# Optimization experiments

Hardware: AMD Instinct MI355X
Metric: run time of the kernel (lower is better)

The kernel has to match this reference:

```python
import jax, jax.numpy as jnp
import numpy as np

NA, NPAP = 50000, 100000
D_IN, D_HID, D_OUT = 512, 512, 256
E_AP, E_PA, E_AA = 400000, 400000, 200000
NEG_SLOPE = 0.2


def setup_inputs() -> dict:
    key = jax.random.key(0)
    ks = jax.random.split(key, 18)
    f32 = jnp.float32

    def edges(k, e, n_src, n_dst):
        k1, k2 = jax.random.split(k)
        return jnp.stack([
            jax.random.randint(k1, (e,), 0, n_src),
            jax.random.randint(k2, (e,), 0, n_dst),
        ]).astype(jnp.int64)

    return {
        'x_author': jax.random.normal(ks[0], (NA, D_IN), f32),
        'x_paper': jax.random.normal(ks[1], (NPAP, D_IN), f32),
        # layer 1 params
        'W1': jax.random.normal(ks[2], (2, D_IN, D_HID), f32) / np.sqrt(D_IN),
        'b1': jnp.zeros((2, D_HID), f32),
        'att1': jax.random.normal(ks[3], (3, 2, D_HID), f32) * 0.1,
        'kW1': jax.random.normal(ks[4], (D_HID, D_HID), f32) / np.sqrt(D_HID),
        'kb1': jnp.zeros((D_HID,), f32),
        'q1': jax.random.normal(ks[5], (D_HID,), f32) * 0.1,
        # layer 2 params
        'W2': jax.random.normal(ks[6], (2, D_HID, D_OUT), f32) / np.sqrt(D_HID),
        'b2': jnp.zeros((2, D_OUT), f32),
        'att2': jax.random.normal(ks[7], (3, 2, D_OUT), f32) * 0.1,
        'kW2': jax.random.normal(ks[8], (D_OUT, D_OUT), f32) / np.sqrt(D_OUT),
        'kb2': jnp.zeros((D_OUT,), f32),
        'q2': jax.random.normal(ks[9], (D_OUT,), f32) * 0.1,
        # edge index dict: (author,writes,paper), (paper,written_by,author), (author,coauthor,author)
        'e_ap': edges(ks[10], E_AP, NA, NPAP),
        'e_pa': edges(ks[11], E_PA, NPAP, NA),
        'e_aa': edges(ks[12], E_AA, NA, NA),
    }


def _edge_type_attn(h_src, h_dst, a_src, a_dst, ei, n_dst):
    """One edge-type GAT-style aggregation of HANConv (heads=1)."""
    src, dst = ei[0], ei[1]
    alpha = (h_src @ a_src)[src] + (h_dst @ a_dst)[dst]        # [E]
    alpha = jax.nn.leaky_relu(alpha, NEG_SLOPE)
    m = jax.ops.segment_max(alpha, dst, num_segments=n_dst)    # softmax over dst groups
    e = jnp.exp(alpha - m[dst])
    denom = jax.ops.segment_sum(e, dst, num_segments=n_dst)
    w = e / denom[dst]                                          # [E]
    out = jax.ops.segment_sum(h_src[src] * w[:, None], dst, num_segments=n_dst)
    return jax.nn.relu(out)                                     # [n_dst, D]


def _semantic_group(outs, kW, kb, q):
    """outs: [T, N, D]; semantic attention over T metapaths."""
    score = jnp.einsum('tnd,d->t', jnp.tanh(outs @ kW + kb), q) / outs.shape[1]
    attn = jax.nn.softmax(score)
    return jnp.einsum('t,tnd->nd', attn, outs)


def _han_layer(x_a, x_p, W, b, att, kW, kb, q, e_ap, e_pa, e_aa):
    h_a = x_a @ W[0] + b[0]   # per-node-type projection
    h_p = x_p @ W[1] + b[1]
    na, npap = h_a.shape[0], h_p.shape[0]
    out_p = _edge_type_attn(h_a, h_p, att[0, 0], att[0, 1], e_ap, npap)
    out_a1 = _edge_type_attn(h_p, h_a, att[1, 0], att[1, 1], e_pa, na)
    out_a2 = _edge_type_attn(h_a, h_a, att[2, 0], att[2, 1], e_aa, na)
    out_a = _semantic_group(jnp.stack([out_a1, out_a2]), kW, kb, q)
    out_p = _semantic_group(out_p[None], kW, kb, q)
    return out_a, out_p


def reference(x_author, x_paper, W1, b1, att1, kW1, kb1, q1,
              W2, b2, att2, kW2, kb2, q2, e_ap, e_pa, e_aa):
    h_a, h_p = _han_layer(x_author, x_paper, W1, b1, att1, kW1, kb1, q1, e_ap, e_pa, e_aa)
    h_a, h_p = _han_layer(h_a, h_p, W2, b2, att2, kW2, kb2, q2, e_ap, e_pa, e_aa)
    return h_a  # x['author']
```

## Files before the change

kernel.cpp:

```cpp
#include <hip/hip_runtime.h>
#include <hip/hip_bf16.h>

#define NA 50000
#define NPAP 100000
#define DIN 512
#define DHID 512
#define DOUT 256
#define EAP 400000
#define EPA 400000
#define EAA 200000

typedef unsigned short u16;
typedef __attribute__((ext_vector_type(8))) short bf16x8;
typedef __attribute__((ext_vector_type(4))) float f32x4;

__device__ inline float bflo(unsigned v) { return __uint_as_float(v << 16); }
__device__ inline float bfhi(unsigned v) { return __uint_as_float(v & 0xffff0000u); }
__device__ inline u16 f2bf_rne(float x) {
    unsigned u = __float_as_uint(x);
    return (u16)((u + 0x7FFFu + ((u >> 16) & 1u)) >> 16);
}
__device__ inline unsigned pack2bf(float a, float b) {
    return (unsigned)f2bf_rne(a) | ((unsigned)f2bf_rne(b) << 16);
}


__global__ void fill_u32_kernel(unsigned* __restrict__ p, unsigned v, int n) {
    int i = blockIdx.x * blockDim.x + threadIdx.x;
    if (i < n) p[i] = v;
}

__global__ void detect_kernel(const unsigned* __restrict__ e, int npairs, int* __restrict__ flag) {
    __shared__ int anyn;
    if (threadIdx.x == 0) anyn = 0;
    __syncthreads();
    unsigned local = 0;
    for (int i = threadIdx.x; i < npairs; i += blockDim.x) local |= e[2 * i + 1];
    if (local) atomicOr(&anyn, 1);
    __syncthreads();
    if (threadIdx.x == 0) flag[0] = (anyn == 0) ? 1 : 0;
}

__device__ inline int edge_at(const void* e, size_t idx, int i64) {
    return i64 ? (int)((const long long*)e)[idx] : ((const int*)e)[idx];
}


__global__ void conv_bt_kernel(const float* __restrict__ B, u16* __restrict__ bth,
                               u16* __restrict__ btl, int K, int N) {
    __shared__ float tile[32][33];
    const int nb = blockIdx.x * 32, kb = blockIdx.y * 32;
    const int tx = threadIdx.x, ty = threadIdx.y;
    const int KBLK = K >> 5;
    for (int i = ty; i < 32; i += 8)
        tile[i][tx] = B[(size_t)(kb + i) * N + nb + tx];
    __syncthreads();
    for (int i = ty; i < 32; i += 8) {
        float v = tile[tx][i];
        unsigned u = __float_as_uint(v);
        unsigned h = (u + 0x7FFFu + ((u >> 16) & 1u)) >> 16;
        float hf = __uint_as_float(h << 16);
        float r = v - hf;
        unsigned l = __float_as_uint(r) >> 16;
        const int n = nb + i, k = kb + tx;
        const int nblk = n >> 7, row = n & 127;
        const int kblk = k >> 5, kc = (k & 31) >> 3, ke = k & 7;
        const int cph = kc ^ ((row >> 1) & 3);
        size_t o = (((size_t)(nblk * KBLK + kblk) * 128 + row) << 5) + (cph << 3) + ke;
        bth[o] = (u16)h;
        btl[o] = (u16)l;
    }
}


template <bool BF16OUT>
__global__ __launch_bounds__(256, 4) void mfma_gemm_2p_kernel(
    const float* __restrict__ A,
    const u16* __restrict__ Bth, const u16* __restrict__ Btl,
    const float* __restrict__ bias,
    float* __restrict__ C, int M, int N, int K, int gx)
{
    __shared__ u16 Ah[128][32];
    __shared__ u16 Bh[128][32];
    __shared__ u16 Bl[128][32];

    const int nwg = gridDim.x;
    const int bid = blockIdx.x;
    const int qc = nwg >> 3, rc = nwg & 7;
    const int xcd = bid & 7, idx = bid >> 3;
    const int wg = (xcd < rc ? xcd * (qc + 1) : rc * (qc + 1) + (xcd - rc) * qc) + idx;
    const int bx = wg % gx, by = wg / gx;
    const int m0 = by * 128;
    const int n0 = bx * 128;

    const int tid = threadIdx.x;
    const int lane = tid & 63;
    const int wv = tid >> 6;
    const int wm = wv >> 1, wn = wv & 1;
    const int fr = lane & 15;
    const int kg = lane >> 4;

    const int srow = tid >> 1;
    const int oh   = tid & 1;
    const bool a_ok = (m0 + srow) < M;
    const float* Ap = A + (size_t)(m0 + srow) * K + oh * 16;

    const int swc = (srow >> 1) & 3;
    const int p0 = srow * 32 + ((((oh << 1) + 0) ^ swc) << 3);
    const int p1 = srow * 32 + ((((oh << 1) + 1) ^ swc) << 3);
    const int rdc = (kg ^ ((fr >> 1) & 3)) << 3;

    const int KBLK = K >> 5;
    const size_t btile0 = ((size_t)(n0 >> 7) * KBLK) << 12;
    const int bso0 = wv * 512 + lane * 8;
    const int bso1 = (wv + 4) * 512 + lane * 8;

    f32x4 acc[4][4] = {};

    const int nt = K >> 5;
    for (int t = 0; t < nt; ++t) {
        __syncthreads();
        {
            const int k0 = t << 5;
            uint4 w0 = make_uint4(0, 0, 0, 0), w1 = w0;
            if (a_ok) {
                float ar[16];
#pragma unroll
                for (int c4 = 0; c4 < 4; ++c4) {
                    float4 v = *(const float4*)(Ap + k0 + c4 * 4);
                    ar[c4 * 4 + 0] = v.x; ar[c4 * 4 + 1] = v.y;
                    ar[c4 * 4 + 2] = v.z; ar[c4 * 4 + 3] = v.w;
                }
                w0 = make_uint4(pack2bf(ar[0], ar[1]), pack2bf(ar[2], ar[3]),
                                pack2bf(ar[4], ar[5]), pack2bf(ar[6], ar[7]));
                w1 = make_uint4(pack2bf(ar[8], ar[9]), pack2bf(ar[10], ar[11]),
                                pack2bf(ar[12], ar[13]), pack2bf(ar[14], ar[15]));
            }
            const u16* bt = Bth + btile0 + ((size_t)t << 12);
            const u16* blt = Btl + btile0 + ((size_t)t << 12);
            uint4 bh0 = *(const uint4*)(bt + bso0);
            uint4 bh1 = *(const uint4*)(bt + bso1);
            uint4 bl0 = *(const uint4*)(blt + bso0);
            uint4 bl1 = *(const uint4*)(blt + bso1);

            u16* ahp = &Ah[0][0];
            *(uint4*)&ahp[p0] = w0;
            *(uint4*)&ahp[p1] = w1;
            u16* bhp = &Bh[0][0];
            u16* blp = &Bl[0][0];
            *(uint4*)&bhp[bso0] = bh0;
            *(uint4*)&bhp[bso1] = bh1;
            *(uint4*)&blp[bso0] = bl0;
            *(uint4*)&blp[bso1] = bl1;
        }
        __syncthreads();

        bf16x8 afh[4], bfh[4], bfl[4];
#pragma unroll
        for (int i = 0; i < 4; ++i) {
            const int aoff = (wm * 64 + i * 16 + fr) * 32 + rdc;
            const int boff = (wn * 64 + i * 16 + fr) * 32 + rdc;
            afh[i] = *(const bf16x8*)&Ah[0][aoff];
            bfh[i] = *(const bf16x8*)&Bh[0][boff];
            bfl[i] = *(const bf16x8*)&Bl[0][boff];
        }
#pragma unroll
        for (int i = 0; i < 4; ++i)
#pragma unroll
            for (int j = 0; j < 4; ++j) {
                acc[i][j] = __builtin_amdgcn_mfma_f32_16x16x32_bf16(afh[i], bfh[j], acc[i][j], 0, 0, 0);
                acc[i][j] = __builtin_amdgcn_mfma_f32_16x16x32_bf16(afh[i], bfl[j], acc[i][j], 0, 0, 0);
            }
    }

#pragma unroll
    for (int j = 0; j < 4; ++j) {
        const int col = n0 + wn * 64 + j * 16 + fr;
        const float bj = bias[col];
#pragma unroll
        for (int i = 0; i < 4; ++i) {
            const int rbase = m0 + wm * 64 + i * 16 + kg * 4;
#pragma unroll
            for (int r = 0; r < 4; ++r) {
                const int grow = rbase + r;
                if (grow < M) {
                    if (BF16OUT)
                        ((u16*)C)[(size_t)grow * N + col] = f2bf_rne(acc[i][j][r] + bj);
                    else
                        C[(size_t)grow * N + col] = acc[i][j][r] + bj;
                }
            }
        }
    }
}


template <bool COMB, bool BF16OUT>
__global__ __launch_bounds__(256, 4) void mfma_gemm_bfA_kernel(
    const u16* __restrict__ A, const u16* __restrict__ A2,
    const float* __restrict__ cwp,
    const u16* __restrict__ Bth, const u16* __restrict__ Btl,
    const float* __restrict__ bias,
    float* __restrict__ C, int M, int N, int K, int gx)
{
    __shared__ u16 Ah[128][32];
    __shared__ u16 Bh[128][32];
    __shared__ u16 Bl[128][32];

    const int nwg = gridDim.x;
    const int bid = blockIdx.x;
    const int qc = nwg >> 3, rc = nwg & 7;
    const int xcd = bid & 7, idx = bid >> 3;
    const int wg = (xcd < rc ? xcd * (qc + 1) : rc * (qc + 1) + (xcd - rc) * qc) + idx;
    const int bx = wg % gx, by = wg / gx;
    const int m0 = by * 128;
    const int n0 = bx * 128;

    const int tid = threadIdx.x;
    const int lane = tid & 63;
    const int wv = tid >> 6;
    const int wm = wv >> 1, wn = wv & 1;
    const int fr = lane & 15;
    const int kg = lane >> 4;

    const int srow = tid >> 1;
    const int oh   = tid & 1;
    const bool a_ok = (m0 + srow) < M;
    const u16* Ap  = A + (size_t)(m0 + srow) * K + oh * 16;
    const u16* Ap2 = COMB ? (A2 + (size_t)(m0 + srow) * K + oh * 16) : nullptr;
    float cw0 = 1.f, cw1 = 0.f;
    if (COMB) { cw0 = cwp[0]; cw1 = cwp[1]; }

    const int swc = (srow >> 1) & 3;
    const int p0 = srow * 32 + ((((oh << 1) + 0) ^ swc) << 3);
    const int p1 = srow * 32 + ((((oh << 1) + 1) ^ swc) << 3);
    const int rdc = (kg ^ ((fr >> 1) & 3)) << 3;

    const int KBLK = K >> 5;
    const size_t btile0 = ((size_t)(n0 >> 7) * KBLK) << 12;
    const int bso0 = wv * 512 + lane * 8;
    const int bso1 = (wv + 4) * 512 + lane * 8;

    f32x4 acc[4][4] = {};

    const int nt = K >> 5;
    for (int t = 0; t < nt; ++t) {
        __syncthreads();
        {
            const int k0 = t << 5;
            uint4 a0 = make_uint4(0, 0, 0, 0), a1 = a0;
            if (a_ok) {
                a0 = *(const uint4*)(Ap + k0);
                a1 = *(const uint4*)(Ap + k0 + 8);
                if (COMB) {
                    uint4 c0 = *(const uint4*)(Ap2 + k0);
                    uint4 c1 = *(const uint4*)(Ap2 + k0 + 8);
                    a0.x = pack2bf(cw0 * bflo(a0.x) + cw1 * bflo(c0.x), cw0 * bfhi(a0.x) + cw1 * bfhi(c0.x));
                    a0.y = pack2bf(cw0 * bflo(a0.y) + cw1 * bflo(c0.y), cw0 * bfhi(a0.y) + cw1 * bfhi(c0.y));
                    a0.z = pack2bf(cw0 * bflo(a0.z) + cw1 * bflo(c0.z), cw0 * bfhi(a0.z) + cw1 * bfhi(c0.z));
                    a0.w = pack2bf(cw0 * bflo(a0.w) + cw1 * bflo(c0.w), cw0 * bfhi(a0.w) + cw1 * bfhi(c0.w));
                    a1.x = pack2bf(cw0 * bflo(a1.x) + cw1 * bflo(c1.x), cw0 * bfhi(a1.x) + cw1 * bfhi(c1.x));
                    a1.y = pack2bf(cw0 * bflo(a1.y) + cw1 * bflo(c1.y), cw0 * bfhi(a1.y) + cw1 * bfhi(c1.y));
                    a1.z = pack2bf(cw0 * bflo(a1.z) + cw1 * bflo(c1.z), cw0 * bfhi(a1.z) + cw1 * bfhi(c1.z));
                    a1.w = pack2bf(cw0 * bflo(a1.w) + cw1 * bflo(c1.w), cw0 * bfhi(a1.w) + cw1 * bfhi(c1.w));
                }
            }
            const u16* bt = Bth + btile0 + ((size_t)t << 12);
            const u16* blt = Btl + btile0 + ((size_t)t << 12);
            uint4 bh0 = *(const uint4*)(bt + bso0);
            uint4 bh1 = *(const uint4*)(bt + bso1);
            uint4 bl0 = *(const uint4*)(blt + bso0);
            uint4 bl1 = *(const uint4*)(blt + bso1);

            u16* ahp = &Ah[0][0];
            *(uint4*)&ahp[p0] = a0;
            *(uint4*)&ahp[p1] = a1;
            u16* bhp = &Bh[0][0];
            u16* blp = &Bl[0][0];
            *(uint4*)&bhp[bso0] = bh0;
            *(uint4*)&bhp[bso1] = bh1;
            *(uint4*)&blp[bso0] = bl0;
            *(uint4*)&blp[bso1] = bl1;
        }
        __syncthreads();

        bf16x8 afh[4], bfh[4], bfl[4];
#pragma unroll
        for (int i = 0; i < 4; ++i) {
            const int aoff = (wm * 64 + i * 16 + fr) * 32 + rdc;
            const int boff = (wn * 64 + i * 16 + fr) * 32 + rdc;
            afh[i] = *(const bf16x8*)&Ah[0][aoff];
            bfh[i] = *(const bf16x8*)&Bh[0][boff];
            bfl[i] = *(const bf16x8*)&Bl[0][boff];
        }
#pragma unroll
        for (int i = 0; i < 4; ++i)
#pragma unroll
            for (int j = 0; j < 4; ++j) {
                acc[i][j] = __builtin_amdgcn_mfma_f32_16x16x32_bf16(afh[i], bfh[j], acc[i][j], 0, 0, 0);
                acc[i][j] = __builtin_amdgcn_mfma_f32_16x16x32_bf16(afh[i], bfl[j], acc[i][j], 0, 0, 0);
            }
    }

#pragma unroll
    for (int j = 0; j < 4; ++j) {
        const int col = n0 + wn * 64 + j * 16 + fr;
        const float bj = bias[col];
#pragma unroll
        for (int i = 0; i < 4; ++i) {
            const int rbase = m0 + wm * 64 + i * 16 + kg * 4;
#pragma unroll
            for (int r = 0; r < 4; ++r) {
                const int grow = rbase + r;
                if (grow < M) {
                    if (BF16OUT)
                        ((u16*)C)[(size_t)grow * N + col] = f2bf_rne(acc[i][j][r] + bj);
                    else
                        C[(size_t)grow * N + col] = acc[i][j][r] + bj;
                }
            }
        }
    }
}


template <bool BF16A>
__global__ __launch_bounds__(256, 4) void mfma_score1_kernel(
    const void* __restrict__ A_, const u16* __restrict__ Bth,
    const float* __restrict__ bias, int M, int N, int K,
    const float* __restrict__ qv, float* __restrict__ score, int gx)
{
    __shared__ u16 Ah[128][32];
    __shared__ u16 Bh[128][32];

    const int nwg = gridDim.x;
    const int bid = blockIdx.x;
    const int qc = nwg >> 3, rc = nwg & 7;
    const int xcd = bid & 7, idx = bid >> 3;
    const int wg = (xcd < rc ? xcd * (qc + 1) : rc * (qc + 1) + (xcd - rc) * qc) + idx;
    const int bx = wg % gx, by = wg / gx;
    const int m0 = by * 128;
    const int n0 = bx * 128;

    const int tid = threadIdx.x;
    const int lane = tid & 63;
    const int wv = tid >> 6;
    const int wm = wv >> 1, wn = wv & 1;
    const int fr = lane & 15;
    const int kg = lane >> 4;

    const int srow = tid >> 1;
    const int oh   = tid & 1;
    const bool a_ok = (m0 + srow) < M;

    const int swc = (srow >> 1) & 3;
    const int p0 = srow * 32 + ((((oh << 1) + 0) ^ swc) << 3);
    const int p1 = srow * 32 + ((((oh << 1) + 1) ^ swc) << 3);
    const int rdc = (kg ^ ((fr >> 1) & 3)) << 3;

    const int KBLK = K >> 5;
    const size_t btile0 = ((size_t)(n0 >> 7) * KBLK) << 12;
    const int bso0 = wv * 512 + lane * 8;
    const int bso1 = (wv + 4) * 512 + lane * 8;

    f32x4 acc[4][4] = {};

    const int nt = K >> 5;
    for (int t = 0; t < nt; ++t) {
        __syncthreads();
        {
            const int k0 = t << 5;
            uint4 w0 = make_uint4(0, 0, 0, 0), w1 = w0;
            if (a_ok) {
                if (BF16A) {
                    const u16* Ap = (const u16*)A_ + (size_t)(m0 + srow) * K + oh * 16;
                    w0 = *(const uint4*)(Ap + k0);
                    w1 = *(const uint4*)(Ap + k0 + 8);
                } else {
                    const float* Ap = (const float*)A_ + (size_t)(m0 + srow) * K + oh * 16;
                    float ar[16];
#pragma unroll
                    for (int c4 = 0; c4 < 4; ++c4) {
                        float4 v = *(const float4*)(Ap + k0 + c4 * 4);
                        ar[c4 * 4 + 0] = v.x; ar[c4 * 4 + 1] = v.y;
                        ar[c4 * 4 + 2] = v.z; ar[c4 * 4 + 3] = v.w;
                    }
                    w0 = make_uint4(pack2bf(ar[0], ar[1]), pack2bf(ar[2], ar[3]),
                                    pack2bf(ar[4], ar[5]), pack2bf(ar[6], ar[7]));
                    w1 = make_uint4(pack2bf(ar[8], ar[9]), pack2bf(ar[10], ar[11]),
                                    pack2bf(ar[12], ar[13]), pack2bf(ar[14], ar[15]));
                }
            }
            const u16* bt = Bth + btile0 + ((size_t)t << 12);
            uint4 bh0 = *(const uint4*)(bt + bso0);
            uint4 bh1 = *(const uint4*)(bt + bso1);
            u16* ahp = &Ah[0][0];
            *(uint4*)&ahp[p0] = w0;
            *(uint4*)&ahp[p1] = w1;
            u16* bhp = &Bh[0][0];
            *(uint4*)&bhp[bso0] = bh0;
            *(uint4*)&bhp[bso1] = bh1;
        }
        __syncthreads();

        bf16x8 afh[4], bfh[4];
#pragma unroll
        for (int i = 0; i < 4; ++i) {
            afh[i] = *(const bf16x8*)&Ah[0][(wm * 64 + i * 16 + fr) * 32 + rdc];
            bfh[i] = *(const bf16x8*)&Bh[0][(wn * 64 + i * 16 + fr) * 32 + rdc];
        }
#pragma unroll
        for (int i = 0; i < 4; ++i)
#pragma unroll
            for (int j = 0; j < 4; ++j)
                acc[i][j] = __builtin_amdgcn_mfma_f32_16x16x32_bf16(afh[i], bfh[j], acc[i][j], 0, 0, 0);
    }

    float ssum = 0.f;
#pragma unroll
    for (int j = 0; j < 4; ++j) {
        const int col = n0 + wn * 64 + j * 16 + fr;
        const float bj = bias[col];
        const float qj = qv[col];
#pragma unroll
        for (int i = 0; i < 4; ++i) {
            const int rbase = m0 + wm * 64 + i * 16 + kg * 4;
#pragma unroll
            for (int r = 0; r < 4; ++r) {
                if (rbase + r < M) ssum += tanhf(acc[i][j][r] + bj) * qj;
            }
        }
    }
#pragma unroll
    for (int o = 32; o; o >>= 1) ssum += __shfl_xor(ssum, o);
    __syncthreads();
    float* red = (float*)&Ah[0][0];
    if (lane == 0) red[wv] = ssum;
    __syncthreads();
    if (tid == 0) atomicAdd(score, red[0] + red[1] + red[2] + red[3]);
}


template <int NV, bool BF16IN>
__global__ void scores_kernel(const void* __restrict__ h, int n, int D,
                              const float* __restrict__ v0, const float* __restrict__ v1,
                              const float* __restrict__ v2, const float* __restrict__ v3,
                              float* __restrict__ s0, float* __restrict__ s1,
                              float* __restrict__ s2, float* __restrict__ s3)
{
    const int lane = threadIdx.x & 63;
    int wid = (blockIdx.x * blockDim.x + threadIdx.x) >> 6;
    const int nw = (gridDim.x * blockDim.x) >> 6;
    for (int node = wid; node < n; node += nw) {
        float a0 = 0, a1 = 0, a2 = 0, a3 = 0;
        for (int d = lane * 4; d < D; d += 256) {
            float4 x;
            if (BF16IN) {
                const u16* row = (const u16*)h + (size_t)node * D;
                uint2 bv = *(const uint2*)&row[d];
                x = make_float4(bflo(bv.x), bfhi(bv.x), bflo(bv.y), bfhi(bv.y));
            } else {
                const float* row = (const float*)h + (size_t)node * D;
                x = *(const float4*)&row[d];
            }
            float4 w = *(const float4*)&v0[d];
            a0 += x.x * w.x + x.y * w.y + x.z * w.z + x.w * w.w;
            if (NV > 1) { float4 u = *(const float4*)&v1[d]; a1 += x.x * u.x + x.y * u.y + x.z * u.z + x.w * u.w; }
            if (NV > 2) { float4 u = *(const float4*)&v2[d]; a2 += x.x * u.x + x.y * u.y + x.z * u.z + x.w * u.w; }
            if (NV > 3) { float4 u = *(const float4*)&v3[d]; a3 += x.x * u.x + x.y * u.y + x.z * u.z + x.w * u.w; }
        }
#pragma unroll
        for (int o = 32; o; o >>= 1) {
            a0 += __shfl_xor(a0, o);
            if (NV > 1) a1 += __shfl_xor(a1, o);
            if (NV > 2) a2 += __shfl_xor(a2, o);
            if (NV > 3) a3 += __shfl_xor(a3, o);
        }
        if (lane == 0) {
            s0[node] = a0;
            if (NV > 1) s1[node] = a1;
            if (NV > 2) s2[node] = a2;
            if (NV > 3) s3[node] = a3;
        }
    }
}


__global__ void count3_kernel(const void* __restrict__ eA, const void* __restrict__ eB,
                              const void* __restrict__ eC, const int* __restrict__ flag,
                              int* __restrict__ cA, int* __restrict__ cB, int* __restrict__ cC) {
    int i = blockIdx.x * blockDim.x + threadIdx.x;
    int f = *flag;
    if (i < EAP) {
        atomicAdd(&cA[edge_at(eA, (size_t)EAP + i, f)], 1);
    } else if (i < EAP + EPA) {
        int j = i - EAP;
        atomicAdd(&cB[edge_at(eB, (size_t)EPA + j, f)], 1);
    } else if (i < EAP + EPA + EAA) {
        int j = i - EAP - EPA;
        atomicAdd(&cC[edge_at(eC, (size_t)EAA + j, f)], 1);
    }
}


__global__ void scanp1_kernel(const int* __restrict__ cnt, int n, int* __restrict__ part) {
    __shared__ int wsum[16];
    const int base = blockIdx.x * 1024;
    const int t = threadIdx.x, lane = t & 63, w = t >> 6;
    int v = (base + t < n) ? cnt[base + t] : 0;
#pragma unroll
    for (int o = 1; o < 64; o <<= 1) v += __shfl_xor(v, o);
    if (lane == 0) wsum[w] = v;
    __syncthreads();
    if (t == 0) {
        int s = 0;
#pragma unroll
        for (int k = 0; k < 16; ++k) s += wsum[k];
        part[blockIdx.x] = s;
    }
}

__global__ void scanp2_kernel(int* __restrict__ part, int nblk) {
    __shared__ int wsum[16];
    const int t = threadIdx.x, lane = t & 63, w = t >> 6;
    int v = (t < nblk) ? part[t] : 0;
    int x = v;
#pragma unroll
    for (int o = 1; o < 64; o <<= 1) { int y = __shfl_up(x, o); if (lane >= o) x += y; }
    if (lane == 63) wsum[w] = x;
    __syncthreads();
    if (w == 0 && lane < 16) {
        int s = wsum[lane];
#pragma unroll
        for (int o = 1; o < 16; o <<= 1) { int y = __shfl_up(s, o); if (lane >= o) s += y; }
        wsum[lane] = s;
    }
    __syncthreads();
    const int woff = (w > 0) ? wsum[w - 1] : 0;
    if (t < nblk) part[t] = woff + x - v;
}

__global__ void scanp3_kernel(const int* __restrict__ cnt, int n, const int* __restrict__ part,
                              int* __restrict__ offs_ap, int* __restrict__ cur_ap,
                              int* __restrict__ offs_pa, int* __restrict__ cur_pa,
                              int* __restrict__ offs_aa, int* __restrict__ cur_aa) {
    __shared__ int wsum[16];
    const int base = blockIdx.x * 1024;
    const int t = threadIdx.x, lane = t & 63, w = t >> 6;
    int v = (base + t < n) ? cnt[base + t] : 0;
    int x = v;
#pragma unroll
    for (int o = 1; o < 64; o <<= 1) { int y = __shfl_up(x, o); if (lane >= o) x += y; }
    if (lane == 63) wsum[w] = x;
    __syncthreads();
    if (w == 0 && lane < 16) {
        int s = wsum[lane];
#pragma unroll
        for (int o = 1; o < 16; o <<= 1) { int y = __shfl_up(s, o); if (lane >= o) s += y; }
        wsum[lane] = s;
    }
    __syncthreads();
    const int woff = (w > 0) ? wsum[w - 1] : 0;
    const int g = part[blockIdx.x] + woff + x - v;
    const int i = base + t;
    if (i < n) {
        if (i < NPAP)                 { offs_ap[i] = g; cur_ap[i] = g; }
        else if (i == NPAP)           { offs_ap[NPAP] = g; }
        else if (i < NPAP + 1 + NA)   { int j = i - NPAP - 1; int val = g - EAP; offs_pa[j] = val; cur_pa[j] = val; }
        else if (i == NPAP + 1 + NA)  { offs_pa[NA] = g - EAP; }
        else if (i < NPAP + 2 + 2*NA) { int j = i - NPAP - NA - 2; int val = g - EAP - EPA; offs_aa[j] = val; cur_aa[j] = val; }
        else                          { offs_aa[NA] = g - EAP - EPA; }
    }
}

__global__ void scatter3_kernel(const void* __restrict__ eA, const void* __restrict__ eB,
                                const void* __restrict__ eC, const int* __restrict__ flag,
                                int* __restrict__ uA, int* __restrict__ uB, int* __restrict__ uC,
                                int* __restrict__ idA, int* __restrict__ idB, int* __restrict__ idC) {
    int i = blockIdx.x * blockDim.x + threadIdx.x;
    int f = *flag;
    if (i < EAP) {
        int d = edge_at(eA, (size_t)EAP + i, f);
        idA[atomicAdd(&uA[d], 1)] = i;
    } else if (i < EAP + EPA) {
        int j = i - EAP;
        int d = edge_at(eB, (size_t)EPA + j, f);
        idB[atomicAdd(&uB[d], 1)] = j;
    } else if (i < EAP + EPA + EAA) {
        int j = i - EAP - EPA;
        int d = edge_at(eC, (size_t)EAA + j, f);
        idC[atomicAdd(&uC[d], 1)] = j;
    }
}


template <int DW, bool BF16H, bool BF16OUT>
__global__ __launch_bounds__(256) void agg_fused_kernel(
    const int* __restrict__ offs, const int* __restrict__ eids,
    const void* __restrict__ e, const int* __restrict__ flag,
    const float* __restrict__ ssrc, const float* __restrict__ sdst,
    const void* __restrict__ hsrc_, void* __restrict__ out,
    int n_dst, int E, int D)
{
    const int lane = threadIdx.x & 63;
    int wid = (blockIdx.x * blockDim.x + threadIdx.x) >> 6;
    const int nw = (gridDim.x * blockDim.x) >> 6;
    const int f = *flag;
    for (int dst = wid; dst < n_dst; dst += nw) {
        const int beg = offs[dst], end = offs[dst + 1];
        const float sd = sdst[dst];

        float dsum = 0.f;
        for (int j = beg + lane; j < end; j += 64) {
            int eid = eids[j];
            float a = ssrc[edge_at(e, eid, f)] + sd;
            a = (a >= 0.f) ? a : 0.2f * a;
            dsum += expf(a);
        }
#pragma unroll
        for (int o = 32; o; o >>= 1) dsum += __shfl_xor(dsum, o);
        const float rden = (end > beg) ? 1.f / dsum : 0.f;

        float acc[DW] = {};
        int j = beg;
        for (; j + 4 <= end; j += 4) {
            const int e0 = eids[j], e1 = eids[j + 1], e2 = eids[j + 2], e3 = eids[j + 3];
            const int q0 = edge_at(e, e0, f), q1 = edge_at(e, e1, f);
            const int q2 = edge_at(e, e2, f), q3 = edge_at(e, e3, f);
            float a0 = ssrc[q0] + sd, a1 = ssrc[q1] + sd;
            float a2 = ssrc[q2] + sd, a3 = ssrc[q3] + sd;
            a0 = (a0 >= 0.f) ? a0 : 0.2f * a0;
            a1 = (a1 >= 0.f) ? a1 : 0.2f * a1;
            a2 = (a2 >= 0.f) ? a2 : 0.2f * a2;
            a3 = (a3 >= 0.f) ? a3 : 0.2f * a3;
            const float w0 = expf(a0) * rden, w1 = expf(a1) * rden;
            const float w2 = expf(a2) * rden, w3 = expf(a3) * rden;
            if (BF16H) {
                const u16* hb = (const u16*)hsrc_;
                const u16* r0 = hb + (size_t)q0 * D + lane * DW;
                const u16* r1 = hb + (size_t)q1 * D + lane * DW;
                const u16* r2 = hb + (size_t)q2 * D + lane * DW;
                const u16* r3 = hb + (size_t)q3 * D + lane * DW;
                if constexpr (DW >= 8) {
#pragma unroll
                    for (int c = 0; c < DW; c += 8) {
                        uint4 b0 = *(const uint4*)&r0[c];
                        uint4 b1 = *(const uint4*)&r1[c];
                        uint4 b2 = *(const uint4*)&r2[c];
                        uint4 b3 = *(const uint4*)&r3[c];
                        acc[c + 0] += bflo(b0.x) * w0 + bflo(b1.x) * w1 + bflo(b2.x) * w2 + bflo(b3.x) * w3;
                        acc[c + 1] += bfhi(b0.x) * w0 + bfhi(b1.x) * w1 + bfhi(b2.x) * w2 + bfhi(b3.x) * w3;
                        acc[c + 2] += bflo(b0.y) * w0 + bflo(b1.y) * w1 + bflo(b2.y) * w2 + bflo(b3.y) * w3;
                        acc[c + 3] += bfhi(b0.y) * w0 + bfhi(b1.y) * w1 + bfhi(b2.y) * w2 + bfhi(b3.y) * w3;
                        acc[c + 4] += bflo(b0.z) * w0 + bflo(b1.z) * w1 + bflo(b2.z) * w2 + bflo(b3.z) * w3;
                        acc[c + 5] += bfhi(b0.z) * w0 + bfhi(b1.z) * w1 + bfhi(b2.z) * w2 + bfhi(b3.z) * w3;
                        acc[c + 6] += bflo(b0.w) * w0 + bflo(b1.w) * w1 + bflo(b2.w) * w2 + bflo(b3.w) * w3;
                        acc[c + 7] += bfhi(b0.w) * w0 + bfhi(b1.w) * w1 + bfhi(b2.w) * w2 + bfhi(b3.w) * w3;
                    }
                } else {
                    uint2 b0 = *(const uint2*)r0;
                    uint2 b1 = *(const uint2*)r1;
                    uint2 b2 = *(const uint2*)r2;
                    uint2 b3 = *(const uint2*)r3;
                    acc[0] += bflo(b0.x) * w0 + bflo(b1.x) * w1 + bflo(b2.x) * w2 + bflo(b3.x) * w3;
                    acc[1] += bfhi(b0.x) * w0 + bfhi(b1.x) * w1 + bfhi(b2.x) * w2 + bfhi(b3.x) * w3;
                    acc[2] += bflo(b0.y) * w0 + bflo(b1.y) * w1 + bflo(b2.y) * w2 + bflo(b3.y) * w3;
                    acc[3] += bfhi(b0.y) * w0 + bfhi(b1.y) * w1 + bfhi(b2.y) * w2 + bfhi(b3.y) * w3;
                }
            } else {
                const float* hf = (const float*)hsrc_;
                const float* r0 = hf + (size_t)q0 * D + lane * DW;
                const float* r1 = hf + (size_t)q1 * D + lane * DW;
                const float* r2 = hf + (size_t)q2 * D + lane * DW;
                const float* r3 = hf + (size_t)q3 * D + lane * DW;
#pragma unroll
                for (int c = 0; c < DW; c += 4) {
                    float4 a0v = *(const float4*)&r0[c];
                    float4 a1v = *(const float4*)&r1[c];
                    float4 a2v = *(const float4*)&r2[c];
                    float4 a3v = *(const float4*)&r3[c];
                    acc[c + 0] += a0v.x * w0 + a1v.x * w1 + a2v.x * w2 + a3v.x * w3;
                    acc[c + 1] += a0v.y * w0 + a1v.y * w1 + a2v.y * w2 + a3v.y * w3;
                    acc[c + 2] += a0v.z * w0 + a1v.z * w1 + a2v.z * w2 + a3v.z * w3;
                    acc[c + 3] += a0v.w * w0 + a1v.w * w1 + a2v.w * w2 + a3v.w * w3;
                }
            }
        }
        for (; j < end; ++j) {
            const int eid = eids[j];
            const int q = edge_at(e, eid, f);
            float a = ssrc[q] + sd;
            a = (a >= 0.f) ? a : 0.2f * a;
            const float w = expf(a) * rden;
            if (BF16H) {
                const u16* row = (const u16*)hsrc_ + (size_t)q * D + lane * DW;
                if constexpr (DW >= 8) {
#pragma unroll
                    for (int c = 0; c < DW; c += 8) {
                        uint4 b0 = *(const uint4*)&row[c];
                        acc[c + 0] += bflo(b0.x) * w; acc[c + 1] += bfhi(b0.x) * w;
                        acc[c + 2] += bflo(b0.y) * w; acc[c + 3] += bfhi(b0.y) * w;
                        acc[c + 4] += bflo(b0.z) * w; acc[c + 5] += bfhi(b0.z) * w;
                        acc[c + 6] += bflo(b0.w) * w; acc[c + 7] += bfhi(b0.w) * w;
                    }
                } else {
                    uint2 b0 = *(const uint2*)row;
                    acc[0] += bflo(b0.x) * w; acc[1] += bfhi(b0.x) * w;
                    acc[2] += bflo(b0.y) * w; acc[3] += bfhi(b0.y) * w;
                }
            } else {
                const float* row = (const float*)hsrc_ + (size_t)q * D + lane * DW;
#pragma unroll
                for (int c = 0; c < DW; c += 4) {
                    float4 v = *(const float4*)&row[c];
                    acc[c + 0] += v.x * w; acc[c + 1] += v.y * w;
                    acc[c + 2] += v.z * w; acc[c + 3] += v.w * w;
                }
            }
        }
        if (BF16OUT) {
            u16* orow = (u16*)out + (size_t)dst * D + lane * DW;
            if constexpr (DW >= 8) {
#pragma unroll
                for (int c = 0; c < DW; c += 8) {
                    uint4 v;
                    v.x = pack2bf(fmaxf(acc[c + 0], 0.f), fmaxf(acc[c + 1], 0.f));
                    v.y = pack2bf(fmaxf(acc[c + 2], 0.f), fmaxf(acc[c + 3], 0.f));
                    v.z = pack2bf(fmaxf(acc[c + 4], 0.f), fmaxf(acc[c + 5], 0.f));
                    v.w = pack2bf(fmaxf(acc[c + 6], 0.f), fmaxf(acc[c + 7], 0.f));
                    *(uint4*)&orow[c] = v;
                }
            } else {
                uint2 v;
                v.x = pack2bf(fmaxf(acc[0], 0.f), fmaxf(acc[1], 0.f));
                v.y = pack2bf(fmaxf(acc[2], 0.f), fmaxf(acc[3], 0.f));
                *(uint2*)orow = v;
            }
        } else {
            float* orow = (float*)out + (size_t)dst * D + lane * DW;
#pragma unroll
            for (int c = 0; c < DW; c += 4) {
                float4 v = make_float4(fmaxf(acc[c + 0], 0.f), fmaxf(acc[c + 1], 0.f),
                                       fmaxf(acc[c + 2], 0.f), fmaxf(acc[c + 3], 0.f));
                *(float4*)&orow[c] = v;
            }
        }
    }
}


__global__ void softmax2_kernel(const float* __restrict__ score, float invN, float* __restrict__ w) {
    if (threadIdx.x == 0 && blockIdx.x == 0) {
        float s0 = score[0] * invN, s1 = score[1] * invN;
        float m = fmaxf(s0, s1);
        float e0 = expf(s0 - m), e1 = expf(s1 - m);
        float r = 1.f / (e0 + e1);
        w[0] = e0 * r;
        w[1] = e1 * r;
    }
}

__global__ void combine2_kernel(const float4* __restrict__ a, const float4* __restrict__ b,
                                const float* __restrict__ w, float4* __restrict__ o, int n4) {
    float w0 = w[0], w1 = w[1];
    for (int i = blockIdx.x * blockDim.x + threadIdx.x; i < n4; i += gridDim.x * blockDim.x) {
        float4 x = a[i], y = b[i];
        o[i] = make_float4(w0 * x.x + w1 * y.x, w0 * x.y + w1 * y.y,
                           w0 * x.z + w1 * y.z, w0 * x.w + w1 * y.w);
    }
}


extern "C" void kernel_launch(void* const* d_in, const int* in_sizes, int n_in,
                              void* d_out, int out_size, void* d_ws, size_t ws_size,
                              hipStream_t stream) {
    const float* x_a  = (const float*)d_in[0];
    const float* x_p  = (const float*)d_in[1];
    const float* W1   = (const float*)d_in[2];
    const float* b1   = (const float*)d_in[3];
    const float* att1 = (const float*)d_in[4];
    const float* kW1  = (const float*)d_in[5];
    const float* kb1  = (const float*)d_in[6];
    const float* q1   = (const float*)d_in[7];
    const float* W2   = (const float*)d_in[8];
    const float* b2   = (const float*)d_in[9];
    const float* att2 = (const float*)d_in[10];
    const float* kW2  = (const float*)d_in[11];
    const float* kb2  = (const float*)d_in[12];
    const float* q2   = (const float*)d_in[13];
    const void* e_ap  = d_in[14];
    const void* e_pa  = d_in[15];
    const void* e_aa  = d_in[16];
    float* out = (float*)d_out;

    size_t off = 0;
    auto ALLOC = [&](size_t nbytes) -> void* {
        void* p = (char*)d_ws + off;
        off += (nbytes + 255) & ~(size_t)255;
        return p;
    };
    float* bufA = (float*)ALLOC((size_t)NPAP * DHID * 4);
    float* bufB = (float*)ALLOC((size_t)NA * DHID * 4);
    float* bufC = (float*)ALLOC((size_t)NA * DHID * 4);
    float* bufD = (float*)ALLOC((size_t)NA * DHID * 4);
    float* sa_w  = (float*)ALLOC((size_t)NA * 4);
    float* sa_pd = (float*)ALLOC((size_t)NA * 4);
    float* sa_as = (float*)ALLOC((size_t)NA * 4);
    float* sa_ad = (float*)ALLOC((size_t)NA * 4);
    float* sp_wd = (float*)ALLOC((size_t)NPAP * 4);
    float* sp_ps = (float*)ALLOC((size_t)NPAP * 4);
    int* cnt3    = (int*)ALLOC((size_t)(NPAP + 2 * NA + 8) * 4);
    int* scanpart = (int*)ALLOC(256 * 4);
    int* cursor3 = (int*)ALLOC((size_t)(NPAP + 2 * NA + 8) * 4);
    int* offs_ap = (int*)ALLOC((size_t)(NPAP + 1) * 4);
    int* offs_pa = (int*)ALLOC((size_t)(NA + 1) * 4);
    int* offs_aa = (int*)ALLOC((size_t)(NA + 1) * 4);
    int* eids_ap = (int*)ALLOC((size_t)EAP * 4);
    int* eids_pa = (int*)ALLOC((size_t)EPA * 4);
    int* eids_aa = (int*)ALLOC((size_t)EAA * 4);
    const size_t WTOT = 262144u * 3 + 131072u * 2 + 65536u;
    u16* w_hi = (u16*)ALLOC(WTOT * 2);
    u16* w_lo = (u16*)ALLOC(WTOT * 2);
    float* score = (float*)ALLOC(8 * 4);
    float* wsem  = (float*)ALLOC(2 * 4);
    int* eflag   = (int*)ALLOC(4);
    if (off > ws_size) return;

    const size_t oW1a = 0, oW1p = 262144, okW1 = 524288;
    const size_t oW2a = 786432, oW2p = 917504, okW2 = 1048576;

    int* cntA = cnt3;
    int* cntB = cnt3 + NPAP + 1;
    int* cntC = cntB + NA + 1;
    int* curA = cursor3;
    int* curB = cursor3 + NPAP + 1;
    int* curC = curB + NA + 1;
    const int CNT3N = NPAP + 2 * NA + 3;

    hipStream_t s = stream;

    detect_kernel<<<1, 256, 0, s>>>((const unsigned*)e_ap, 1024, eflag);

    auto conv_b = [&](const float* B_, int K, int N, size_t wo) {
        conv_bt_kernel<<<dim3(N / 32, K / 32), dim3(32, 8), 0, s>>>(B_, w_hi + wo, w_lo + wo, K, N);
    };
    conv_b(W1, DIN, DHID, oW1a);
    conv_b(W1 + (size_t)DIN * DHID, DIN, DHID, oW1p);
    conv_b(kW1, DHID, DHID, okW1);
    conv_b(W2, DHID, DOUT, oW2a);
    conv_b(W2 + (size_t)DHID * DOUT, DHID, DOUT, oW2p);
    conv_b(kW2, DOUT, DOUT, okW2);

    {
        const int ETOT = EAP + EPA + EAA;
        const int nblk = (CNT3N + 1023) / 1024;
        fill_u32_kernel<<<(CNT3N + 255) / 256, 256, 0, s>>>((unsigned*)cnt3, 0u, CNT3N);
        count3_kernel<<<(ETOT + 255) / 256, 256, 0, s>>>(e_ap, e_pa, e_aa, eflag, cntA, cntB, cntC);
        scanp1_kernel<<<nblk, 1024, 0, s>>>(cnt3, CNT3N, scanpart);
        scanp2_kernel<<<1, 1024, 0, s>>>(scanpart, nblk);
        scanp3_kernel<<<nblk, 1024, 0, s>>>(cnt3, CNT3N, scanpart,
                                            offs_ap, curA, offs_pa, curB, offs_aa, curC);
        scatter3_kernel<<<(ETOT + 255) / 256, 256, 0, s>>>(e_ap, e_pa, e_aa, eflag,
                                                           curA, curB, curC,
                                                           eids_ap, eids_pa, eids_aa);
    }

    auto gemm_proj_h = [&](const float* A_, size_t wo, const float* bias_, float* C_,
                           int M, int N, int K) {
        int gx = N / 128;
        int nwg = gx * ((M + 127) / 128);
        mfma_gemm_2p_kernel<true><<<nwg, 256, 0, s>>>(A_,
            w_hi + wo, w_lo + wo, bias_, C_, M, N, K, gx);
    };
    auto gemm_proj_bfA_h = [&](const u16* A_, size_t wo, const float* bias_, float* C_,
                               int M, int N, int K) {
        int gx = N / 128;
        int nwg = gx * ((M + 127) / 128);
        mfma_gemm_bfA_kernel<false, true><<<nwg, 256, 0, s>>>(A_, nullptr, nullptr,
            w_hi + wo, w_lo + wo, bias_, C_, M, N, K, gx);
    };
    auto gemm_proj_bfA_comb_h = [&](const u16* A_, const u16* A2_, const float* cw, size_t wo,
                                    const float* bias_, float* C_, int M, int N, int K) {
        int gx = N / 128;
        int nwg = gx * ((M + 127) / 128);
        mfma_gemm_bfA_kernel<true, true><<<nwg, 256, 0, s>>>(A_, A2_, cw,
            w_hi + wo, w_lo + wo, bias_, C_, M, N, K, gx);
    };
    auto gemm_score_b = [&](const void* A_, size_t wo, const float* bias_, int M, int N, int K,
                            const float* qv, float* sc) {
        int gx = N / 128;
        int nwg = gx * ((M + 127) / 128);
        mfma_score1_kernel<true><<<nwg, 256, 0, s>>>(A_, w_hi + wo, bias_, M, N, K, qv, sc, gx);
    };
    auto gemm_score_f = [&](const void* A_, size_t wo, const float* bias_, int M, int N, int K,
                            const float* qv, float* sc) {
        int gx = N / 128;
        int nwg = gx * ((M + 127) / 128);
        mfma_score1_kernel<false><<<nwg, 256, 0, s>>>(A_, w_hi + wo, bias_, M, N, K, qv, sc, gx);
    };

    u16* h_a = (u16*)bufB;
    u16* h_p = (u16*)bufA;
    gemm_proj_h(x_a, oW1a, b1, (float*)h_a, NA, DHID, DIN);
    gemm_proj_h(x_p, oW1p, b1 + DHID, (float*)h_p, NPAP, DHID, DIN);

    {
        int ga = (NA + 3) / 4 < 4096 ? (NA + 3) / 4 : 4096;
        int gp = (NPAP + 3) / 4 < 4096 ? (NPAP + 3) / 4 : 4096;
        scores_kernel<4, true><<<ga, 256, 0, s>>>(h_a, NA, DHID,
            att1 + 0 * DHID, att1 + 3 * DHID, att1 + 4 * DHID, att1 + 5 * DHID,
            sa_w, sa_pd, sa_as, sa_ad);
        scores_kernel<2, true><<<gp, 256, 0, s>>>(h_p, NPAP, DHID,
            att1 + 1 * DHID, att1 + 2 * DHID, nullptr, nullptr,
            sp_wd, sp_ps, nullptr, nullptr);
    }

    u16* o1  = (u16*)bufC;
    u16* o2  = (u16*)bufD;
    u16* x2p = (u16*)bufA + (size_t)NPAP * DHID;
    {
        int gw = (NA + 3) / 4;
        agg_fused_kernel<8, true, true><<<gw, 256, 0, s>>>(offs_pa, eids_pa, e_pa, eflag,
            sp_ps, sa_pd, h_p, o1, NA, EPA, DHID);
        agg_fused_kernel<8, true, true><<<gw, 256, 0, s>>>(offs_aa, eids_aa, e_aa, eflag,
            sa_as, sa_ad, h_a, o2, NA, EAA, DHID);
        int gw2 = (NPAP + 3) / 4;
        agg_fused_kernel<8, true, true><<<gw2, 256, 0, s>>>(offs_ap, eids_ap, e_ap, eflag,
            sa_w, sp_wd, h_a, x2p, NPAP, EAP, DHID);
    }

    fill_u32_kernel<<<1, 64, 0, s>>>((unsigned*)score, 0u, 2);
    gemm_score_b(o1, okW1, kb1, NA, DHID, DHID, q1, &score[0]);
    gemm_score_b(o2, okW1, kb1, NA, DHID, DHID, q1, &score[1]);
    softmax2_kernel<<<1, 64, 0, s>>>(score, 1.f / (float)NA, wsem);

    u16* h2a = (u16*)bufB;
    u16* h2p = (u16*)bufD;
    gemm_proj_bfA_comb_h(o1, o2, wsem, oW2a, b2, (float*)h2a, NA, DOUT, DHID);
    gemm_proj_bfA_h(x2p, oW2p, b2 + DOUT, (float*)h2p, NPAP, DOUT, DHID);

    {
        int ga = (NA + 3) / 4 < 4096 ? (NA + 3) / 4 : 4096;
        int gp = (NPAP + 3) / 4 < 4096 ? (NPAP + 3) / 4 : 4096;
        scores_kernel<3, true><<<ga, 256, 0, s>>>(h2a, NA, DOUT,
            att2 + 3 * DOUT, att2 + 4 * DOUT, att2 + 5 * DOUT, nullptr,
            sa_pd, sa_as, sa_ad, nullptr);
        scores_kernel<1, true><<<gp, 256, 0, s>>>(h2p, NPAP, DOUT,
            att2 + 2 * DOUT, nullptr, nullptr, nullptr,
            sp_ps, nullptr, nullptr, nullptr);
    }

    float* oa1 = bufC;
    float* oa2 = bufC + (size_t)NA * DOUT;
    {
        int gw = (NA + 3) / 4;
        agg_fused_kernel<4, true, false><<<gw, 256, 0, s>>>(offs_pa, eids_pa, e_pa, eflag,
            sp_ps, sa_pd, h2p, oa1, NA, EPA, DOUT);
        agg_fused_kernel<4, true, false><<<gw, 256, 0, s>>>(offs_aa, eids_aa, e_aa, eflag,
            sa_as, sa_ad, h2a, oa2, NA, EAA, DOUT);
    }

    fill_u32_kernel<<<1, 64, 0, s>>>((unsigned*)score, 0u, 2);
    gemm_score_f(oa1, okW2, kb2, NA, DOUT, DOUT, q2, &score[0]);
    gemm_score_f(oa2, okW2, kb2, NA, DOUT, DOUT, q2, &score[1]);
    softmax2_kernel<<<1, 64, 0, s>>>(score, 1.f / (float)NA, wsem);
    combine2_kernel<<<2048, 256, 0, s>>>((const float4*)oa1, (const float4*)oa2, wsem,
                                         (float4*)out, NA * DOUT / 4);
}
```

Baseline: 1.242 ms.

## Register-prefetch next K tile in MFMA GEMM kernels to overlap loads with compute

Restructures the main loop of the three MFMA GEMM kernels so the global loads for tile t+1 are issued into registers right after the LDS stores of tile t, before its MFMAs run. This hides global memory latency behind the matrix-core work instead of stalling at the start of each iteration. The cost is extra live registers, so the launch-bounds occupancy hint is lowered from 4 to 3 workgroups per CU, which may reduce latency hiding across waves.

```diff
diff --git a/kernel.cpp b/kernel.cpp
--- a/kernel.cpp
+++ b/kernel.cpp
@@ -74,7 +74,7 @@
 
 
 template <bool BF16OUT>
-__global__ __launch_bounds__(256, 4) void mfma_gemm_2p_kernel(
+__global__ __launch_bounds__(256, 3) void mfma_gemm_2p_kernel(
     const float* __restrict__ A,
     const u16* __restrict__ Bth, const u16* __restrict__ Btl,
     const float* __restrict__ bias,
@@ -117,43 +117,53 @@
 
     f32x4 acc[4][4] = {};
 
+    float ar[16];
+    uint4 rbh0, rbh1, rbl0, rbl1;
+
+    auto loadregs = [&](int t) {
+        const int k0 = t << 5;
+        if (a_ok) {
+#pragma unroll
+            for (int c4 = 0; c4 < 4; ++c4) {
+                float4 v = *(const float4*)(Ap + k0 + c4 * 4);
+                ar[c4 * 4 + 0] = v.x; ar[c4 * 4 + 1] = v.y;
+                ar[c4 * 4 + 2] = v.z; ar[c4 * 4 + 3] = v.w;
+            }
+        } else {
+#pragma unroll
+            for (int c = 0; c < 16; ++c) ar[c] = 0.f;
+        }
+        const u16* bt  = Bth + btile0 + ((size_t)t << 12);
+        const u16* blt = Btl + btile0 + ((size_t)t << 12);
+        rbh0 = *(const uint4*)(bt + bso0);
+        rbh1 = *(const uint4*)(bt + bso1);
+        rbl0 = *(const uint4*)(blt + bso0);
+        rbl1 = *(const uint4*)(blt + bso1);
+    };
+
+    auto storeregs = [&]() {
+        uint4 w0 = make_uint4(pack2bf(ar[0], ar[1]), pack2bf(ar[2], ar[3]),
+                              pack2bf(ar[4], ar[5]), pack2bf(ar[6], ar[7]));
+        uint4 w1 = make_uint4(pack2bf(ar[8], ar[9]), pack2bf(ar[10], ar[11]),
+                              pack2bf(ar[12], ar[13]), pack2bf(ar[14], ar[15]));
+        u16* ahp = &Ah[0][0];
+        *(uint4*)&ahp[p0] = w0;
+        *(uint4*)&ahp[p1] = w1;
+        u16* bhp = &Bh[0][0];
+        u16* blp = &Bl[0][0];
+        *(uint4*)&bhp[bso0] = rbh0;
+        *(uint4*)&bhp[bso1] = rbh1;
+        *(uint4*)&blp[bso0] = rbl0;
+        *(uint4*)&blp[bso1] = rbl1;
+    };
+
+    loadregs(0);
     const int nt = K >> 5;
     for (int t = 0; t < nt; ++t) {
         __syncthreads();
-        {
-            const int k0 = t << 5;
-            uint4 w0 = make_uint4(0, 0, 0, 0), w1 = w0;
-            if (a_ok) {
-                float ar[16];
-#pragma unroll
-                for (int c4 = 0; c4 < 4; ++c4) {
-                    float4 v = *(const float4*)(Ap + k0 + c4 * 4);
-                    ar[c4 * 4 + 0] = v.x; ar[c4 * 4 + 1] = v.y;
-                    ar[c4 * 4 + 2] = v.z; ar[c4 * 4 + 3] = v.w;
-                }
-                w0 = make_uint4(pack2bf(ar[0], ar[1]), pack2bf(ar[2], ar[3]),
-                                pack2bf(ar[4], ar[5]), pack2bf(ar[6], ar[7]));
-                w1 = make_uint4(pack2bf(ar[8], ar[9]), pack2bf(ar[10], ar[11]),
-                                pack2bf(ar[12], ar[13]), pack2bf(ar[14], ar[15]));
-            }
-            const u16* bt = Bth + btile0 + ((size_t)t << 12);
-            const u16* blt = Btl + btile0 + ((size_t)t << 12);
-            uint4 bh0 = *(const uint4*)(bt + bso0);
-            uint4 bh1 = *(const uint4*)(bt + bso1);
-            uint4 bl0 = *(const uint4*)(blt + bso0);
-            uint4 bl1 = *(const uint4*)(blt + bso1);
-
-            u16* ahp = &Ah[0][0];
-            *(uint4*)&ahp[p0] = w0;
-            *(uint4*)&ahp[p1] = w1;
-            u16* bhp = &Bh[0][0];
-            u16* blp = &Bl[0][0];
-            *(uint4*)&bhp[bso0] = bh0;
-            *(uint4*)&bhp[bso1] = bh1;
-            *(uint4*)&blp[bso0] = bl0;
-            *(uint4*)&blp[bso1] = bl1;
-        }
+        storeregs();
         __syncthreads();
+        if (t + 1 < nt) loadregs(t + 1);
 
         bf16x8 afh[4], bfh[4], bfl[4];
 #pragma unroll
@@ -196,7 +206,7 @@
 
 
 template <bool COMB, bool BF16OUT>
-__global__ __launch_bounds__(256, 4) void mfma_gemm_bfA_kernel(
+__global__ __launch_bounds__(256, 3) void mfma_gemm_bfA_kernel(
     const u16* __restrict__ A, const u16* __restrict__ A2,
     const float* __restrict__ cwp,
     const u16* __restrict__ Bth, const u16* __restrict__ Btl,
@@ -243,46 +253,60 @@
 
     f32x4 acc[4][4] = {};
 
+    uint4 a0r, a1r, c0r, c1r;
+    uint4 rbh0, rbh1, rbl0, rbl1;
+
+    auto loadregs = [&](int t) {
+        const int k0 = t << 5;
+        a0r = make_uint4(0, 0, 0, 0); a1r = a0r;
+        if (a_ok) {
+            a0r = *(const uint4*)(Ap + k0);
+            a1r = *(const uint4*)(Ap + k0 + 8);
+            if (COMB) {
+                c0r = *(const uint4*)(Ap2 + k0);
+                c1r = *(const uint4*)(Ap2 + k0 + 8);
+            }
+        } else if (COMB) {
+            c0r = make_uint4(0, 0, 0, 0); c1r = c0r;
+        }
+        const u16* bt  = Bth + btile0 + ((size_t)t << 12);
+        const u16* blt = Btl + btile0 + ((size_t)t << 12);
+        rbh0 = *(const uint4*)(bt + bso0);
+        rbh1 = *(const uint4*)(bt + bso1);
+        rbl0 = *(const uint4*)(blt + bso0);
+        rbl1 = *(const uint4*)(blt + bso1);
+    };
+
+    auto storeregs = [&]() {
+        uint4 a0 = a0r, a1 = a1r;
+        if (COMB) {
+            a0.x = pack2bf(cw0 * bflo(a0r.x) + cw1 * bflo(c0r.x), cw0 * bfhi(a0r.x) + cw1 * bfhi(c0r.x));
+            a0.y = pack2bf(cw0 * bflo(a0r.y) + cw1 * bflo(c0r.y), cw0 * bfhi(a0r.y) + cw1 * bfhi(c0r.y));
+            a0.z = pack2bf(cw0 * bflo(a0r.z) + cw1 * bflo(c0r.z), cw0 * bfhi(a0r.z) + cw1 * bfhi(c0r.z));
+            a0.w = pack2bf(cw0 * bflo(a0r.w) + cw1 * bflo(c0r.w), cw0 * bfhi(a0r.w) + cw1 * bfhi(c0r.w));
+            a1.x = pack2bf(cw0 * bflo(a1r.x) + cw1 * bflo(c1r.x), cw0 * bfhi(a1r.x) + cw1 * bfhi(c1r.x));
+            a1.y = pack2bf(cw0 * bflo(a1r.y) + cw1 * bflo(c1r.y), cw0 * bfhi(a1r.y) + cw1 * bfhi(c1r.y));
+            a1.z = pack2bf(cw0 * bflo(a1r.z) + cw1 * bflo(c1r.z), cw0 * bfhi(a1r.z) + cw1 * bfhi(c1r.z));
+            a1.w = pack2bf(cw0 * bflo(a1r.w) + cw1 * bflo(c1r.w), cw0 * bfhi(a1r.w) + cw1 * bfhi(c1r.w));
+        }
+        u16* ahp = &Ah[0][0];
+        *(uint4*)&ahp[p0] = a0;
+        *(uint4*)&ahp[p1] = a1;
+        u16* bhp = &Bh[0][0];
+        u16* blp = &Bl[0][0];
+        *(uint4*)&bhp[bso0] = rbh0;
+        *(uint4*)&bhp[bso1] = rbh1;
+        *(uint4*)&blp[bso0] = rbl0;
+        *(uint4*)&blp[bso1] = rbl1;
+    };
+
+    loadregs(0);
     const int nt = K >> 5;
     for (int t = 0; t < nt; ++t) {
         __syncthreads();
-        {
-            const int k0 = t << 5;
-            uint4 a0 = make_uint4(0, 0, 0, 0), a1 = a0;
-            if (a_ok) {
-                a0 = *(const uint4*)(Ap + k0);
-                a1 = *(const uint4*)(Ap + k0 + 8);
-                if (COMB) {
-                    uint4 c0 = *(const uint4*)(Ap2 + k0);
-                    uint4 c1 = *(const uint4*)(Ap2 + k0 + 8);
-                    a0.x = pack2bf(cw0 * bflo(a0.x) + cw1 * bflo(c0.x), cw0 * bfhi(a0.x) + cw1 * bfhi(c0.x));
-                    a0.y = pack2bf(cw0 * bflo(a0.y) + cw1 * bflo(c0.y), cw0 * bfhi(a0.y) + cw1 * bfhi(c0.y));
-                    a0.z = pack2bf(cw0 * bflo(a0.z) + cw1 * bflo(c0.z), cw0 * bfhi(a0.z) + cw1 * bfhi(c0.z));
-                    a0.w = pack2bf(cw0 * bflo(a0.w) + cw1 * bflo(c0.w), cw0 * bfhi(a0.w) + cw1 * bfhi(c0.w));
-                    a1.x = pack2bf(cw0 * bflo(a1.x) + cw1 * bflo(c1.x), cw0 * bfhi(a1.x) + cw1 * bfhi(c1.x));
-                    a1.y = pack2bf(cw0 * bflo(a1.y) + cw1 * bflo(c1.y), cw0 * bfhi(a1.y) + cw1 * bfhi(c1.y));
-                    a1.z = pack2bf(cw0 * bflo(a1.z) + cw1 * bflo(c1.z), cw0 * bfhi(a1.z) + cw1 * bfhi(c1.z));
-                    a1.w = pack2bf(cw0 * bflo(a1.w) + cw1 * bflo(c1.w), cw0 * bfhi(a1.w) + cw1 * bfhi(c1.w));
-                }
-            }
-            const u16* bt = Bth + btile0 + ((size_t)t << 12);
-            const u16* blt = Btl + btile0 + ((size_t)t << 12);
-            uint4 bh0 = *(const uint4*)(bt + bso0);
-            uint4 bh1 = *(const uint4*)(bt + bso1);
-            uint4 bl0 = *(const uint4*)(blt + bso0);
-            uint4 bl1 = *(const uint4*)(blt + bso1);
-
-            u16* ahp = &Ah[0][0];
-            *(uint4*)&ahp[p0] = a0;
-            *(uint4*)&ahp[p1] = a1;
-            u16* bhp = &Bh[0][0];
-            u16* blp = &Bl[0][0];
-            *(uint4*)&bhp[bso0] = bh0;
-            *(uint4*)&bhp[bso1] = bh1;
-            *(uint4*)&blp[bso0] = bl0;
-            *(uint4*)&blp[bso1] = bl1;
-        }
+        storeregs();
         __syncthreads();
+        if (t + 1 < nt) loadregs(t + 1);
 
         bf16x8 afh[4], bfh[4], bfl[4];
 #pragma unroll
@@ -325,7 +349,7 @@
 
 
 template <bool BF16A>
-__global__ __launch_bounds__(256, 4) void mfma_score1_kernel(
+__global__ __launch_bounds__(256, 3) void mfma_score1_kernel(
     const void* __restrict__ A_, const u16* __restrict__ Bth,
     const float* __restrict__ bias, int M, int N, int K,
     const float* __restrict__ qv, float* __restrict__ score, int gx)
@@ -365,43 +389,62 @@
 
     f32x4 acc[4][4] = {};
 
+    float arf[16];
+    uint4 w0r, w1r;
+    uint4 rbh0, rbh1;
+
+    auto loadregs = [&](int t) {
+        const int k0 = t << 5;
+        if (a_ok) {
+            if (BF16A) {
+                const u16* Ap = (const u16*)A_ + (size_t)(m0 + srow) * K + oh * 16;
+                w0r = *(const uint4*)(Ap + k0);
+                w1r = *(const uint4*)(Ap + k0 + 8);
+            } else {
+                const float* Ap = (const float*)A_ + (size_t)(m0 + srow) * K + oh * 16;
+#pragma unroll
+                for (int c4 = 0; c4 < 4; ++c4) {
+                    float4 v = *(const float4*)(Ap + k0 + c4 * 4);
+                    arf[c4 * 4 + 0] = v.x; arf[c4 * 4 + 1] = v.y;
+                    arf[c4 * 4 + 2] = v.z; arf[c4 * 4 + 3] = v.w;
+                }
+            }
+        } else {
+            if (BF16A) { w0r = make_uint4(0, 0, 0, 0); w1r = w0r; }
+            else {
+#pragma unroll
+                for (int c = 0; c < 16; ++c) arf[c] = 0.f;
+            }
+        }
+        const u16* bt = Bth + btile0 + ((size_t)t << 12);
+        rbh0 = *(const uint4*)(bt + bso0);
+        rbh1 = *(const uint4*)(bt + bso1);
+    };
+
+    auto storeregs = [&]() {
+        uint4 w0, w1;
+        if (BF16A) { w0 = w0r; w1 = w1r; }
+        else {
+            w0 = make_uint4(pack2bf(arf[0], arf[1]), pack2bf(arf[2], arf[3]),
+                            pack2bf(arf[4], arf[5]), pack2bf(arf[6], arf[7]));
+            w1 = make_uint4(pack2bf(arf[8], arf[9]), pack2bf(arf[10], arf[11]),
+                            pack2bf(arf[12], arf[13]), pack2bf(arf[14], arf[15]));
+        }
+        u16* ahp = &Ah[0][0];
+        *(uint4*)&ahp[p0] = w0;
+        *(uint4*)&ahp[p1] = w1;
+        u16* bhp = &Bh[0][0];
+        *(uint4*)&bhp[bso0] = rbh0;
+        *(uint4*)&bhp[bso1] = rbh1;
+    };
+
+    loadregs(0);
     const int nt = K >> 5;
     for (int t = 0; t < nt; ++t) {
         __syncthreads();
-        {
-            const int k0 = t << 5;
-            uint4 w0 = make_uint4(0, 0, 0, 0), w1 = w0;
-            if (a_ok) {
-                if (BF16A) {
-                    const u16* Ap = (const u16*)A_ + (size_t)(m0 + srow) * K + oh * 16;
-                    w0 = *(const uint4*)(Ap + k0);
-                    w1 = *(const uint4*)(Ap + k0 + 8);
-                } else {
-                    const float* Ap = (const float*)A_ + (size_t)(m0 + srow) * K + oh * 16;
-                    float ar[16];
-#pragma unroll
-                    for (int c4 = 0; c4 < 4; ++c4) {
-                        float4 v = *(const float4*)(Ap + k0 + c4 * 4);
-                        ar[c4 * 4 + 0] = v.x; ar[c4 * 4 + 1] = v.y;
-                        ar[c4 * 4 + 2] = v.z; ar[c4 * 4 + 3] = v.w;
-                    }
-                    w0 = make_uint4(pack2bf(ar[0], ar[1]), pack2bf(ar[2], ar[3]),
-                                    pack2bf(ar[4], ar[5]), pack2bf(ar[6], ar[7]));
-                    w1 = make_uint4(pack2bf(ar[8], ar[9]), pack2bf(ar[10], ar[11]),
-                                    pack2bf(ar[12], ar[13]), pack2bf(ar[14], ar[15]));
-                }
-            }
-            const u16* bt = Bth + btile0 + ((size_t)t << 12);
-            uint4 bh0 = *(const uint4*)(bt + bso0);
-            uint4 bh1 = *(const uint4*)(bt + bso1);
-            u16* ahp = &Ah[0][0];
-            *(uint4*)&ahp[p0] = w0;
-            *(uint4*)&ahp[p1] = w1;
-            u16* bhp = &Bh[0][0];
-            *(uint4*)&bhp[bso0] = bh0;
-            *(uint4*)&bhp[bso1] = bh1;
-        }
+        storeregs();
         __syncthreads();
+        if (t + 1 < nt) loadregs(t + 1);
 
         bf16x8 afh[4], bfh[4];
 #pragma unroll
```

After: 1.362 ms. 1.1x slower.
